# Optimization experiments

Measured on AMD Instinct MI355X. Metric: run time of the kernel, lower is better.

Reference implementation:

```python
import jax, jax.numpy as jnp
import numpy as np


def setup_inputs() -> dict:
    key = jax.random.key(0)
    k1, k2 = jax.random.split(key)
    B, S, H = 16, 512, 512
    x = jax.random.normal(k1, (B, S, H), dtype=jnp.float32)
    durations = jax.random.randint(k2, (B, S), 0, 16, dtype=jnp.int32)
    return {"x": x, "durations": durations, "max_len": 4096}


def reference(x, durations, max_len):
    # x: [B, S, H] float, durations: [B, S] int, max_len: python int
    B, S, H = x.shape
    # Inclusive cumulative end positions of each token's expanded span.
    cum = jnp.cumsum(durations, axis=1)                      # [B, S]
    t = jnp.arange(max_len, dtype=cum.dtype)                 # [T]
    # For output frame t, source token j is the first with cum[j] > t.
    idx = jax.vmap(lambda c: jnp.searchsorted(c, t, side='right'))(cum)  # [B, T]
    valid = idx < S                                          # frames beyond total stay zero
    idx_c = jnp.minimum(idx, S - 1)
    out = jnp.take_along_axis(x, idx_c[:, :, None], axis=1)  # [B, T, H]
    return jnp.where(valid[:, :, None], out, jnp.zeros((), dtype=x.dtype))
```

## Files before the change

kernel.cpp:

```cpp
#include <hip/hip_runtime.h>
#include <hip/hip_bf16.h>

__global__ void lr_cumsum_kernel(const int* __restrict__ dur, int* __restrict__ cum,
                                 const int* __restrict__ T_ptr, int BS, int BT) {
    const int T = *T_ptr;
    const int B = BT / T;
    const int S = BS / B;
    __shared__ int sdata[1024];
    const int tid = threadIdx.x;
    for (int row = blockIdx.x; row < B; row += gridDim.x) {
        int carry = 0;
        for (int base = 0; base < S; base += 1024) {
            const int n = min(1024, S - base);
            __syncthreads();
            int v = (tid < n) ? dur[row * S + base + tid] : 0;
            sdata[tid] = v;
            __syncthreads();
            #pragma unroll
            for (int off = 1; off < 1024; off <<= 1) {
                int add = (tid >= off) ? sdata[tid - off] : 0;
                __syncthreads();
                sdata[tid] += add;
                __syncthreads();
            }
            if (tid < n) cum[row * S + base + tid] = sdata[tid] + carry;
            carry += sdata[1023];
        }
    }
}

__global__ __launch_bounds__(128)
void lr_expand_kernel(const float4* __restrict__ x, const int* __restrict__ cum,
                      float4* __restrict__ out, const int* __restrict__ T_ptr,
                      int BS, int BT, int H4) {
    const int T = *T_ptr;
    const int bt = blockIdx.x;
    const int b  = bt / T;
    const int t  = bt - b * T;
    const int B  = BT / T;
    const int S  = BS / B;

    const int* __restrict__ c = cum + b * S;
    int lo = 0, hi = S;
    while (lo < hi) {
        int mid = (lo + hi) >> 1;
        if (c[mid] <= t) lo = mid + 1; else hi = mid;
    }
    const bool valid = lo < S;
    const int idx = valid ? lo : (S - 1);

    const float4* __restrict__ src = x + (size_t)(b * S + idx) * H4;
    float4* __restrict__ dst = out + (size_t)bt * H4;
    const float4 zero = make_float4(0.f, 0.f, 0.f, 0.f);
    for (int i = threadIdx.x; i < H4; i += blockDim.x) {
        dst[i] = valid ? src[i] : zero;
    }
}

extern "C" void kernel_launch(void* const* d_in, const int* in_sizes, int n_in,
                              void* d_out, int out_size, void* d_ws, size_t ws_size,
                              hipStream_t stream) {
    const float* x     = (const float*)d_in[0];
    const int*   dur   = (const int*)d_in[1];
    const int*   T_ptr = (const int*)d_in[2];
    float*       out   = (float*)d_out;

    const int BSH = in_sizes[0];
    const int BS  = in_sizes[1];
    const int H   = BSH / BS;
    const int BT  = out_size / H;
    const int H4  = H / 4;

    int* cum = (int*)d_ws;

    lr_cumsum_kernel<<<64, 1024, 0, stream>>>(dur, cum, T_ptr, BS, BT);
    lr_expand_kernel<<<BT, 128, 0, stream>>>((const float4*)x, cum, (float4*)out,
                                             T_ptr, BS, BT, H4);
}
```

Before: 189.9 us.

## Replace per-frame binary-search gather with per-token scatter plus zero-tail kernel

Instead of launching one block per output frame that binary-searches the cumulative durations and gathers a row, the code launches one block per source token, which loads its row once and writes it to every frame in its span. A separate kernel zeroes frames past each batch's total length. The scan block size is also reduced to 512 to match S. The aim is to remove the per-frame search and the repeated reads of x. In exchange it adds a third launch, the zero kernel reads cum once per thread, and the scatter assumes H4 equals the 128-thread block size.

After: 170.6 us. -10.2%, faster.

```diff
diff --git a/kernel.cpp b/kernel.cpp
--- a/kernel.cpp
+++ b/kernel.cpp
@@ -1,59 +1,76 @@
 #include <hip/hip_runtime.h>
 #include <hip/hip_bf16.h>
 
-__global__ void lr_cumsum_kernel(const int* __restrict__ dur, int* __restrict__ cum,
-                                 const int* __restrict__ T_ptr, int BS, int BT) {
+#define SCAN_BLOCK 512
+
+__global__ __launch_bounds__(SCAN_BLOCK)
+void lr_cumsum_kernel(const int* __restrict__ dur, int* __restrict__ cum,
+                      const int* __restrict__ T_ptr, int BS, int BT) {
     const int T = *T_ptr;
     const int B = BT / T;
     const int S = BS / B;
-    __shared__ int sdata[1024];
+    __shared__ int sdata[SCAN_BLOCK];
     const int tid = threadIdx.x;
     for (int row = blockIdx.x; row < B; row += gridDim.x) {
         int carry = 0;
-        for (int base = 0; base < S; base += 1024) {
-            const int n = min(1024, S - base);
+        for (int base = 0; base < S; base += SCAN_BLOCK) {
+            const int n = min(SCAN_BLOCK, S - base);
             __syncthreads();
             int v = (tid < n) ? dur[row * S + base + tid] : 0;
             sdata[tid] = v;
             __syncthreads();
             #pragma unroll
-            for (int off = 1; off < 1024; off <<= 1) {
+            for (int off = 1; off < SCAN_BLOCK; off <<= 1) {
                 int add = (tid >= off) ? sdata[tid - off] : 0;
                 __syncthreads();
                 sdata[tid] += add;
                 __syncthreads();
             }
             if (tid < n) cum[row * S + base + tid] = sdata[tid] + carry;
-            carry += sdata[1023];
+            carry += sdata[SCAN_BLOCK - 1];
         }
     }
 }
 
 __global__ __launch_bounds__(128)
-void lr_expand_kernel(const float4* __restrict__ x, const int* __restrict__ cum,
-                      float4* __restrict__ out, const int* __restrict__ T_ptr,
-                      int BS, int BT, int H4) {
+void lr_scatter_kernel(const float4* __restrict__ x, const int* __restrict__ cum,
+                       float4* __restrict__ out, const int* __restrict__ T_ptr,
+                       int BS, int BT, int H4) {
     const int T = *T_ptr;
-    const int bt = blockIdx.x;
-    const int b  = bt / T;
-    const int t  = bt - b * T;
-    const int B  = BT / T;
-    const int S  = BS / B;
+    const int B = BT / T;
+    const int S = BS / B;
+    const int id = blockIdx.x;
+    const int b  = id / S;
+    const int j  = id - b * S;
 
-    const int* __restrict__ c = cum + b * S;
-    int lo = 0, hi = S;
-    while (lo < hi) {
-        int mid = (lo + hi) >> 1;
-        if (c[mid] <= t) lo = mid + 1; else hi = mid;
+    int end   = cum[id];
+    int start = (j == 0) ? 0 : cum[id - 1];
+    end   = min(end, T);
+    start = min(start, T);
+    if (start >= end) return;
+
+    const float4 v = x[(size_t)id * H4 + threadIdx.x];
+    float4* __restrict__ dst = out + ((size_t)b * T + start) * H4 + threadIdx.x;
+    for (int f = start; f < end; ++f) {
+        *dst = v;
+        dst += H4;
     }
-    const bool valid = lo < S;
-    const int idx = valid ? lo : (S - 1);
+}
 
-    const float4* __restrict__ src = x + (size_t)(b * S + idx) * H4;
-    float4* __restrict__ dst = out + (size_t)bt * H4;
-    const float4 zero = make_float4(0.f, 0.f, 0.f, 0.f);
-    for (int i = threadIdx.x; i < H4; i += blockDim.x) {
-        dst[i] = valid ? src[i] : zero;
+__global__ __launch_bounds__(256)
+void lr_zerotail_kernel(const int* __restrict__ cum, float4* __restrict__ out,
+                        const int* __restrict__ T_ptr, int BS, int BT, int H4) {
+    const int T = *T_ptr;
+    const int B = BT / T;
+    const int S = BS / B;
+    const long long g = (long long)blockIdx.x * blockDim.x + threadIdx.x;
+    const long long frame = g / H4;
+    if (frame >= (long long)BT) return;
+    const int b = (int)(frame / T);
+    const int t = (int)(frame - (long long)b * T);
+    const int total = min(cum[b * S + S - 1], T);
+    if (t >= total) {
+        out[g] = make_float4(0.f, 0.f, 0.f, 0.f);
     }
 }
 
@@ -73,7 +90,10 @@
 
     int* cum = (int*)d_ws;
 
-    lr_cumsum_kernel<<<64, 1024, 0, stream>>>(dur, cum, T_ptr, BS, BT);
-    lr_expand_kernel<<<BT, 128, 0, stream>>>((const float4*)x, cum, (float4*)out,
-                                             T_ptr, BS, BT, H4);
+    lr_cumsum_kernel<<<64, SCAN_BLOCK, 0, stream>>>(dur, cum, T_ptr, BS, BT);
+    lr_scatter_kernel<<<BS, 128, 0, stream>>>((const float4*)x, cum, (float4*)out,
+                                              T_ptr, BS, BT, H4);
+    const long long n4 = (long long)out_size / 4;
+    const int zgrid = (int)((n4 + 255) / 256);
+    lr_zerotail_kernel<<<zgrid, 256, 0, stream>>>(cum, (float4*)out, T_ptr, BS, BT, H4);
 }
```

## Scatter frame-to-token map in scan kernel, flatten expand with nontemporal stores

Applied to the files above, without the earlier changes.

The scan kernel now writes each token's index directly into a per-frame map over its expanded span and fills -1 past the total length. This removes the per-frame binary search from the expand kernel. The expand kernel becomes a flat grid-stride-free copy where each thread handles one float4, looks up its frame's token, and writes with nontemporal stores. The flat indexing assumes H/4 is a power of two, and the scatter loop runs serially per token with up to 15 writes.

Measured after the change: 170.4 us. 1.11x faster.

```diff
diff --git a/kernel.cpp b/kernel.cpp
--- a/kernel.cpp
+++ b/kernel.cpp
@@ -1,60 +1,59 @@
 #include <hip/hip_runtime.h>
 #include <hip/hip_bf16.h>
 
-__global__ void lr_cumsum_kernel(const int* __restrict__ dur, int* __restrict__ cum,
-                                 const int* __restrict__ T_ptr, int BS, int BT) {
+#define SCAN_BLOCK 512
+
+typedef __attribute__((ext_vector_type(4))) float f32x4;
+
+__global__ __launch_bounds__(SCAN_BLOCK)
+void lr_buildmap_kernel(const int* __restrict__ dur, int* __restrict__ map,
+                        const int* __restrict__ T_ptr, int BS, int BT) {
     const int T = *T_ptr;
     const int B = BT / T;
     const int S = BS / B;
-    __shared__ int sdata[1024];
+    __shared__ int sdata[SCAN_BLOCK];
     const int tid = threadIdx.x;
     for (int row = blockIdx.x; row < B; row += gridDim.x) {
         int carry = 0;
-        for (int base = 0; base < S; base += 1024) {
-            const int n = min(1024, S - base);
+        for (int base = 0; base < S; base += SCAN_BLOCK) {
+            const int n = min(SCAN_BLOCK, S - base);
             __syncthreads();
-            int v = (tid < n) ? dur[row * S + base + tid] : 0;
+            const int v = (tid < n) ? dur[row * S + base + tid] : 0;
             sdata[tid] = v;
             __syncthreads();
             #pragma unroll
-            for (int off = 1; off < 1024; off <<= 1) {
+            for (int off = 1; off < SCAN_BLOCK; off <<= 1) {
                 int add = (tid >= off) ? sdata[tid - off] : 0;
                 __syncthreads();
                 sdata[tid] += add;
                 __syncthreads();
             }
-            if (tid < n) cum[row * S + base + tid] = sdata[tid] + carry;
-            carry += sdata[1023];
+            if (tid < n) {
+                const int inc   = sdata[tid] + carry;
+                const int end   = min(inc, T);
+                const int start = min(inc - v, T);
+                const int tok   = row * S + base + tid;
+                for (int t = start; t < end; ++t) map[row * T + t] = tok;
+            }
+            carry += sdata[SCAN_BLOCK - 1];
         }
+        __syncthreads();
+        const int total = min(carry, T);
+        for (int t = total + tid; t < T; t += SCAN_BLOCK) map[row * T + t] = -1;
     }
 }
 
-__global__ __launch_bounds__(128)
-void lr_expand_kernel(const float4* __restrict__ x, const int* __restrict__ cum,
-                      float4* __restrict__ out, const int* __restrict__ T_ptr,
-                      int BS, int BT, int H4) {
-    const int T = *T_ptr;
-    const int bt = blockIdx.x;
-    const int b  = bt / T;
-    const int t  = bt - b * T;
-    const int B  = BT / T;
-    const int S  = BS / B;
-
-    const int* __restrict__ c = cum + b * S;
-    int lo = 0, hi = S;
-    while (lo < hi) {
-        int mid = (lo + hi) >> 1;
-        if (c[mid] <= t) lo = mid + 1; else hi = mid;
-    }
-    const bool valid = lo < S;
-    const int idx = valid ? lo : (S - 1);
-
-    const float4* __restrict__ src = x + (size_t)(b * S + idx) * H4;
-    float4* __restrict__ dst = out + (size_t)bt * H4;
-    const float4 zero = make_float4(0.f, 0.f, 0.f, 0.f);
-    for (int i = threadIdx.x; i < H4; i += blockDim.x) {
-        dst[i] = valid ? src[i] : zero;
-    }
+__global__ __launch_bounds__(256)
+void lr_expand_kernel(const f32x4* __restrict__ x, const int* __restrict__ map,
+                      f32x4* __restrict__ out, int n4, int shift) {
+    const int g = blockIdx.x * blockDim.x + threadIdx.x;
+    if (g >= n4) return;
+    const int frame = g >> shift;
+    const int lane  = g & ((1 << shift) - 1);
+    const int tok   = map[frame];
+    f32x4 v = (f32x4)(0.f, 0.f, 0.f, 0.f);
+    if (tok >= 0) v = x[((size_t)tok << shift) + lane];
+    __builtin_nontemporal_store(v, &out[g]);
 }
 
 extern "C" void kernel_launch(void* const* d_in, const int* in_sizes, int n_in,
@@ -63,17 +62,20 @@
     const float* x     = (const float*)d_in[0];
     const int*   dur   = (const int*)d_in[1];
     const int*   T_ptr = (const int*)d_in[2];
-    float*       out   = (float*)d_out;
 
     const int BSH = in_sizes[0];
     const int BS  = in_sizes[1];
     const int H   = BSH / BS;
     const int BT  = out_size / H;
     const int H4  = H / 4;
+    const int shift = __builtin_ctz(H4);
 
-    int* cum = (int*)d_ws;
+    int* map = (int*)d_ws;
 
-    lr_cumsum_kernel<<<64, 1024, 0, stream>>>(dur, cum, T_ptr, BS, BT);
-    lr_expand_kernel<<<BT, 128, 0, stream>>>((const float4*)x, cum, (float4*)out,
-                                             T_ptr, BS, BT, H4);
+    lr_buildmap_kernel<<<64, SCAN_BLOCK, 0, stream>>>(dur, map, T_ptr, BS, BT);
+
+    const int n4 = out_size / 4;
+    const int grid = (n4 + 255) / 256;
+    lr_expand_kernel<<<grid, 256, 0, stream>>>((const f32x4*)x, map, (f32x4*)d_out,
+                                               n4, shift);
 }
```
